# Optimization experiments

Measured on AMD Instinct MI355X. Metric: run time of the kernel, lower is better.

Reference implementation:

```python
import jax, jax.numpy as jnp
import numpy as np

BETA = 6.0
LOG_2PI = float(np.log(2.0 * np.pi))


def setup_inputs() -> dict:
    key = jax.random.key(0)
    k1, k2, k3, k4 = jax.random.split(key, 4)
    B, L = 2048, 64
    kl = jax.random.uniform(k1, (B, L), dtype=jnp.float32)
    z_mean = jax.random.normal(k2, (B, L), dtype=jnp.float32)
    z_logvar = jax.random.normal(k3, (B, L), dtype=jnp.float32)
    z_sampled = jax.random.normal(k4, (B, L), dtype=jnp.float32)
    return {"kl": kl, "z_mean": z_mean, "z_logvar": z_logvar, "z_sampled": z_sampled}


def gaussian_log_density(samples, mean, log_var):
    # samples: [B,1,L], mean/log_var: [1,B,L] -> [B,B,L]
    tmp = samples - mean
    return -0.5 * (tmp * tmp * jnp.exp(-log_var) + log_var + LOG_2PI)


def total_correlation(z, z_mean, z_logvar):
    # [B, B, L]: log q(z_i_l | x_j)
    log_qz_prob = gaussian_log_density(z[:, None, :], z_mean[None, :, :], z_logvar[None, :, :])
    # sum_l logsumexp_j -> [B]
    log_qz_product = jnp.sum(jax.scipy.special.logsumexp(log_qz_prob, axis=1), axis=1)
    # logsumexp_j sum_l -> [B]
    log_qz = jax.scipy.special.logsumexp(jnp.sum(log_qz_prob, axis=2), axis=1)
    return jnp.mean(log_qz - log_qz_product)


def reference(kl, z_mean, z_logvar, z_sampled):
    kl_loss = jnp.sum(kl)
    tc = (BETA - 1.0) * total_correlation(z_sampled, z_mean, z_logvar)
    return tc + kl_loss
```

## Files before the change

### kernel.cpp

```cpp
#include <hip/hip_runtime.h>
#include <math.h>


#define NB 2048
#define NL 64
#define NE (NB * NL)
#define BVAL 12.0f

__device__ __forceinline__ float wredsum(float v) {
#pragma unroll
  for (int o = 32; o; o >>= 1) v += __shfl_xor(v, o, 64);
  return v;
}
__device__ __forceinline__ float wredmax(float v) {
#pragma unroll
  for (int o = 32; o; o >>= 1) v = fmaxf(v, __shfl_xor(v, o, 64));
  return v;
}

__global__ __launch_bounds__(256) void k1_pre(const float* __restrict__ kl,
                                              const float* __restrict__ zm,
                                              const float* __restrict__ zlv,
                                              float2* __restrict__ PK2A,
                                              float* __restrict__ PK2B,
                                              float* __restrict__ A2T,
                                              float* __restrict__ MA2T,
                                              float* __restrict__ QC2,
                                              float* __restrict__ KLP) {
  const float INVLN2 = 1.4426950408889634f;
  const float LOG2PI = 1.8378770664093453f;
  int tid = threadIdx.x;
  int e = blockIdx.x * 256 + tid;
  int j = e >> 6, l = e & 63;
  float lv = zlv[e], m = zm[e];
  float a2 = -0.5f * INVLN2 * __expf(-lv);
  float b2 = -0.5f * INVLN2 * (lv + LOG2PI);
  float c1 = -2.0f * a2 * m;
  float c0 = fmaf(a2 * m, m, b2);
  PK2A[e] = make_float2(a2, c1);
  PK2B[e] = c0 - BVAL;
  A2T[l * NB + j] = a2;
  MA2T[l * NB + j] = c1;
  float q = wredsum(c0);
  if (l == 0) QC2[j] = q;
  float ks = wredsum(kl[e]);
  __shared__ float sk[4];
  if (l == 0) sk[tid >> 6] = ks;
  __syncthreads();
  if (tid == 0) KLP[blockIdx.x] = sk[0] + sk[1] + sk[2] + sk[3];
}

__global__ __launch_bounds__(256) void k23(const float* __restrict__ zs,
                                           const float* __restrict__ A2T,
                                           const float* __restrict__ MA2T,
                                           const float* __restrict__ QC2,
                                           const float2* __restrict__ PK2A,
                                           const float* __restrict__ PK2B,
                                           float* __restrict__ TPM,
                                           float* __restrict__ TPS,
                                           float* __restrict__ SP) {
  int jc = blockIdx.x;
  int i0 = blockIdx.y * 8;
  int tid = threadIdx.x;
  int w = tid >> 6, l = tid & 63;
  int j = jc * 256 + tid;

  __shared__ float zsh[64][8];
  if (tid < 128) {
    int k = tid >> 1, r0 = (tid & 1) * 4;
#pragma unroll
    for (int r = 0; r < 4; ++r) zsh[k][r0 + r] = zs[(i0 + r0 + r) * NL + k];
  }
  __syncthreads();

  float accv[8];
  float q = QC2[j];
#pragma unroll
  for (int r = 0; r < 8; ++r) accv[r] = q;
  for (int k = 0; k < 64; ++k) {
    float av = A2T[k * NB + j];
    float mv = MA2T[k * NB + j];
    const float4* z4 = (const float4*)&zsh[k][0];
    float4 za = z4[0], zb = z4[1];
    float zk[8] = {za.x, za.y, za.z, za.w, zb.x, zb.y, zb.z, zb.w};
#pragma unroll
    for (int r = 0; r < 8; ++r) {
      accv[r] = fmaf(zk[r] * zk[r], av, accv[r]);
      accv[r] = fmaf(zk[r], mv, accv[r]);
    }
  }
  __shared__ float lm[4][8], ls[4][8];
  float Mt[8];
#pragma unroll
  for (int r = 0; r < 8; ++r) {
    float mx = wredmax(accv[r]);
    if (l == 0) lm[w][r] = mx;
  }
  __syncthreads();
#pragma unroll
  for (int r = 0; r < 8; ++r)
    Mt[r] = fmaxf(fmaxf(lm[0][r], lm[1][r]), fmaxf(lm[2][r], lm[3][r]));
#pragma unroll
  for (int r = 0; r < 8; ++r) {
    float ss = wredsum(__builtin_amdgcn_exp2f(accv[r] - Mt[r]));
    if (l == 0) ls[w][r] = ss;
  }
  __syncthreads();
  if (tid == 0) {
#pragma unroll
    for (int r = 0; r < 8; ++r) {
      TPM[(i0 + r) * 8 + jc] = Mt[r];
      TPS[(i0 + r) * 8 + jc] = ls[0][r] + ls[1][r] + ls[2][r] + ls[3][r];
    }
  }

  float zr[8];
#pragma unroll
  for (int r = 0; r < 8; ++r) zr[r] = zs[(i0 + r) * NL + l];
  float S[8];
#pragma unroll
  for (int r = 0; r < 8; ++r) S[r] = 0.0f;
  const float2* pa = PK2A + (size_t)(jc * 256 + w * 64) * NL + l;
  const float* pb = PK2B + (size_t)(jc * 256 + w * 64) * NL + l;
#pragma unroll 4
  for (int jj = 0; jj < 64; ++jj) {
    float2 c01 = pa[(size_t)jj * NL];
    float c2 = pb[(size_t)jj * NL];
#pragma unroll
    for (int r = 0; r < 8; ++r) {
      float lp2 = fmaf(fmaf(zr[r], c01.x, c01.y), zr[r], c2);
      S[r] += __builtin_amdgcn_exp2f(lp2);
    }
  }
  __shared__ float lss[4][8][64];
#pragma unroll
  for (int r = 0; r < 8; ++r) lss[w][r][l] = S[r];
  __syncthreads();
  for (int pp = tid; pp < 512; pp += 256) {
    int r = pp >> 6, ll = pp & 63;
    float Sc = lss[0][r][ll] + lss[1][r][ll] + lss[2][r][ll] + lss[3][r][ll];
    SP[((size_t)jc * NB + (i0 + r)) * NL + ll] = Sc;
  }
}

__global__ __launch_bounds__(256) void k4_fin(const float* __restrict__ SP,
                                              const float* __restrict__ TPM,
                                              const float* __restrict__ TPS,
                                              float* __restrict__ PERI) {
  int tid = threadIdx.x;
  int w = tid >> 6, l = tid & 63;
  int i = blockIdx.x * 4 + w;
  float S = 0.0f;
#pragma unroll
  for (int s = 0; s < 8; ++s) S += SP[((size_t)s * NB + i) * NL + l];
  float val = __builtin_amdgcn_logf(S);
  float lqp2 = wredsum(val) + 64.0f * BVAL;
  float tm = (l < 8) ? TPM[i * 8 + l] : -1e30f;
  float ts = (l < 8) ? TPS[i * 8 + l] : 0.0f;
  float Mt = wredmax(tm);
  float St = wredsum(ts * __builtin_amdgcn_exp2f(tm - Mt));
  float lqz2 = Mt + __builtin_amdgcn_logf(St);
  if (l == 0) PERI[i] = lqz2 - lqp2;
}

__global__ __launch_bounds__(256) void k5_out(const float* __restrict__ KLP,
                                              const float* __restrict__ PERI,
                                              float* __restrict__ out) {
  int tid = threadIdx.x;
  float a = 0.0f, b = 0.0f;
  for (int x = tid; x < 512; x += 256) a += KLP[x];
  for (int x = tid; x < 2048; x += 256) b += PERI[x];
  float ra = wredsum(a), rb = wredsum(b);
  __shared__ float sa[4], sb[4];
  if ((tid & 63) == 0) {
    sa[tid >> 6] = ra;
    sb[tid >> 6] = rb;
  }
  __syncthreads();
  if (tid == 0) {
    const float LN2 = 0.6931471805599453f;
    float ka = sa[0] + sa[1] + sa[2] + sa[3];
    float kb = sb[0] + sb[1] + sb[2] + sb[3];
    out[0] = ka + 5.0f * LN2 * kb * (1.0f / (float)NB);
  }
}

extern "C" void kernel_launch(void* const* d_in, const int* in_sizes, int n_in,
                              void* d_out, int out_size, void* d_ws, size_t ws_size,
                              hipStream_t stream) {
  const float* kl = (const float*)d_in[0];
  const float* zm = (const float*)d_in[1];
  const float* zlv = (const float*)d_in[2];
  const float* zs = (const float*)d_in[3];
  float* ws = (float*)d_ws;

  float* PK2A = ws;
  float* PK2B = PK2A + 2 * NE;
  float* A2T = PK2B + NE;
  float* MA2T = A2T + NE;
  float* QC2 = MA2T + NE;
  float* SP = QC2 + NB;
  float* TPM = SP + 8 * NE;
  float* TPS = TPM + NB * 8;
  float* KLP = TPS + NB * 8;
  float* PERI = KLP + 512;

  k1_pre<<<NE / 256, 256, 0, stream>>>(kl, zm, zlv, (float2*)PK2A, PK2B, A2T,
                                       MA2T, QC2, KLP);
  k23<<<dim3(8, NB / 8), 256, 0, stream>>>(zs, A2T, MA2T, QC2,
                                           (const float2*)PK2A, PK2B, TPM, TPS,
                                           SP);
  k4_fin<<<NB / 4, 256, 0, stream>>>(SP, TPM, TPS, PERI);
  k5_out<<<1, 256, 0, stream>>>(KLP, PERI, (float*)d_out);
}
```

Baseline: 130.2 us.

## Split fused k23 into two block roles and pack transposed coefficients as float2

```diff
diff --git a/kernel.cpp b/kernel.cpp
--- a/kernel.cpp
+++ b/kernel.cpp
@@ -23,8 +23,7 @@
                                               const float* __restrict__ zlv,
                                               float2* __restrict__ PK2A,
                                               float* __restrict__ PK2B,
-                                              float* __restrict__ A2T,
-                                              float* __restrict__ MA2T,
+                                              float2* __restrict__ AM2T,
                                               float* __restrict__ QC2,
                                               float* __restrict__ KLP) {
   const float INVLN2 = 1.4426950408889634f;
@@ -39,8 +38,7 @@
   float c0 = fmaf(a2 * m, m, b2);
   PK2A[e] = make_float2(a2, c1);
   PK2B[e] = c0 - BVAL;
-  A2T[l * NB + j] = a2;
-  MA2T[l * NB + j] = c1;
+  AM2T[l * NB + j] = make_float2(a2, c1);
   float q = wredsum(c0);
   if (l == 0) QC2[j] = q;
   float ks = wredsum(kl[e]);
@@ -51,8 +49,7 @@
 }
 
 __global__ __launch_bounds__(256) void k23(const float* __restrict__ zs,
-                                           const float* __restrict__ A2T,
-                                           const float* __restrict__ MA2T,
+                                           const float2* __restrict__ AM2T,
                                            const float* __restrict__ QC2,
                                            const float2* __restrict__ PK2A,
                                            const float* __restrict__ PK2B,
@@ -60,86 +57,87 @@
                                            float* __restrict__ TPS,
                                            float* __restrict__ SP) {
   int jc = blockIdx.x;
-  int i0 = blockIdx.y * 8;
+  int y = blockIdx.y;
+  int i0 = (y >> 1) * 8;
   int tid = threadIdx.x;
   int w = tid >> 6, l = tid & 63;
-  int j = jc * 256 + tid;
-
-  __shared__ float zsh[64][8];
-  if (tid < 128) {
-    int k = tid >> 1, r0 = (tid & 1) * 4;
-#pragma unroll
-    for (int r = 0; r < 4; ++r) zsh[k][r0 + r] = zs[(i0 + r0 + r) * NL + k];
-  }
-  __syncthreads();
-
-  float accv[8];
-  float q = QC2[j];
-#pragma unroll
-  for (int r = 0; r < 8; ++r) accv[r] = q;
-  for (int k = 0; k < 64; ++k) {
-    float av = A2T[k * NB + j];
-    float mv = MA2T[k * NB + j];
-    const float4* z4 = (const float4*)&zsh[k][0];
-    float4 za = z4[0], zb = z4[1];
-    float zk[8] = {za.x, za.y, za.z, za.w, zb.x, zb.y, zb.z, zb.w};
+
+  if ((y & 1) == 0) {
+    int j = jc * 256 + tid;
+    __shared__ float zsh[64][8];
+    if (tid < 128) {
+      int k = tid >> 1, r0 = (tid & 1) * 4;
+#pragma unroll
+      for (int r = 0; r < 4; ++r) zsh[k][r0 + r] = zs[(i0 + r0 + r) * NL + k];
+    }
+    __syncthreads();
+    float accv[8];
+    float q = QC2[j];
+#pragma unroll
+    for (int r = 0; r < 8; ++r) accv[r] = q;
+    for (int k = 0; k < 64; ++k) {
+      float2 am = AM2T[k * NB + j];
+      const float4* z4 = (const float4*)&zsh[k][0];
+      float4 za = z4[0], zb = z4[1];
+      float zk[8] = {za.x, za.y, za.z, za.w, zb.x, zb.y, zb.z, zb.w};
+#pragma unroll
+      for (int r = 0; r < 8; ++r) {
+        accv[r] = fmaf(zk[r] * zk[r], am.x, accv[r]);
+        accv[r] = fmaf(zk[r], am.y, accv[r]);
+      }
+    }
+    __shared__ float lm[4][8], ls[4][8];
+    float Mt[8];
 #pragma unroll
     for (int r = 0; r < 8; ++r) {
-      accv[r] = fmaf(zk[r] * zk[r], av, accv[r]);
-      accv[r] = fmaf(zk[r], mv, accv[r]);
-    }
-  }
-  __shared__ float lm[4][8], ls[4][8];
-  float Mt[8];
-#pragma unroll
-  for (int r = 0; r < 8; ++r) {
-    float mx = wredmax(accv[r]);
-    if (l == 0) lm[w][r] = mx;
-  }
-  __syncthreads();
-#pragma unroll
-  for (int r = 0; r < 8; ++r)
-    Mt[r] = fmaxf(fmaxf(lm[0][r], lm[1][r]), fmaxf(lm[2][r], lm[3][r]));
-#pragma unroll
-  for (int r = 0; r < 8; ++r) {
-    float ss = wredsum(__builtin_amdgcn_exp2f(accv[r] - Mt[r]));
-    if (l == 0) ls[w][r] = ss;
-  }
-  __syncthreads();
-  if (tid == 0) {
+      float mx = wredmax(accv[r]);
+      if (l == 0) lm[w][r] = mx;
+    }
+    __syncthreads();
+#pragma unroll
+    for (int r = 0; r < 8; ++r)
+      Mt[r] = fmaxf(fmaxf(lm[0][r], lm[1][r]), fmaxf(lm[2][r], lm[3][r]));
 #pragma unroll
     for (int r = 0; r < 8; ++r) {
-      TPM[(i0 + r) * 8 + jc] = Mt[r];
-      TPS[(i0 + r) * 8 + jc] = ls[0][r] + ls[1][r] + ls[2][r] + ls[3][r];
-    }
-  }
-
-  float zr[8];
-#pragma unroll
-  for (int r = 0; r < 8; ++r) zr[r] = zs[(i0 + r) * NL + l];
-  float S[8];
-#pragma unroll
-  for (int r = 0; r < 8; ++r) S[r] = 0.0f;
-  const float2* pa = PK2A + (size_t)(jc * 256 + w * 64) * NL + l;
-  const float* pb = PK2B + (size_t)(jc * 256 + w * 64) * NL + l;
+      float ss = wredsum(__builtin_amdgcn_exp2f(accv[r] - Mt[r]));
+      if (l == 0) ls[w][r] = ss;
+    }
+    __syncthreads();
+    if (tid == 0) {
+#pragma unroll
+      for (int r = 0; r < 8; ++r) {
+        TPM[(i0 + r) * 8 + jc] = Mt[r];
+        TPS[(i0 + r) * 8 + jc] = ls[0][r] + ls[1][r] + ls[2][r] + ls[3][r];
+      }
+    }
+  } else {
+    float zr[8];
+#pragma unroll
+    for (int r = 0; r < 8; ++r) zr[r] = zs[(i0 + r) * NL + l];
+    float S[8];
+#pragma unroll
+    for (int r = 0; r < 8; ++r) S[r] = 0.0f;
+    const float2* pa = PK2A + (size_t)(jc * 256 + w * 64) * NL + l;
+    const float* pb = PK2B + (size_t)(jc * 256 + w * 64) * NL + l;
 #pragma unroll 4
-  for (int jj = 0; jj < 64; ++jj) {
-    float2 c01 = pa[(size_t)jj * NL];
-    float c2 = pb[(size_t)jj * NL];
-#pragma unroll
-    for (int r = 0; r < 8; ++r) {
-      float lp2 = fmaf(fmaf(zr[r], c01.x, c01.y), zr[r], c2);
-      S[r] += __builtin_amdgcn_exp2f(lp2);
-    }
-  }
-  __shared__ float lss[4][8][64];
-#pragma unroll
-  for (int r = 0; r < 8; ++r) lss[w][r][l] = S[r];
-  __syncthreads();
-  for (int pp = tid; pp < 512; pp += 256) {
-    int r = pp >> 6, ll = pp & 63;
-    float Sc = lss[0][r][ll] + lss[1][r][ll] + lss[2][r][ll] + lss[3][r][ll];
-    SP[((size_t)jc * NB + (i0 + r)) * NL + ll] = Sc;
+    for (int jj = 0; jj < 64; ++jj) {
+      float2 c01 = pa[(size_t)jj * NL];
+      float c2 = pb[(size_t)jj * NL];
+#pragma unroll
+      for (int r = 0; r < 8; ++r) {
+        float lp2 = fmaf(fmaf(zr[r], c01.x, c01.y), zr[r], c2);
+        S[r] += __builtin_amdgcn_exp2f(lp2);
+      }
+    }
+    __shared__ float lss[4][8][64];
+#pragma unroll
+    for (int r = 0; r < 8; ++r) lss[w][r][l] = S[r];
+    __syncthreads();
+    for (int pp = tid; pp < 512; pp += 256) {
+      int r = pp >> 6, ll = pp & 63;
+      float Sc = lss[0][r][ll] + lss[1][r][ll] + lss[2][r][ll] + lss[3][r][ll];
+      SP[((size_t)jc * NB + (i0 + r)) * NL + ll] = Sc;
+    }
   }
 }
 
@@ -196,20 +194,19 @@
 
   float* PK2A = ws;
   float* PK2B = PK2A + 2 * NE;
-  float* A2T = PK2B + NE;
-  float* MA2T = A2T + NE;
-  float* QC2 = MA2T + NE;
+  float* AM2T = PK2B + NE;
+  float* QC2 = AM2T + 2 * NE;
   float* SP = QC2 + NB;
   float* TPM = SP + 8 * NE;
   float* TPS = TPM + NB * 8;
   float* KLP = TPS + NB * 8;
   float* PERI = KLP + 512;
 
-  k1_pre<<<NE / 256, 256, 0, stream>>>(kl, zm, zlv, (float2*)PK2A, PK2B, A2T,
-                                       MA2T, QC2, KLP);
-  k23<<<dim3(8, NB / 8), 256, 0, stream>>>(zs, A2T, MA2T, QC2,
-                                           (const float2*)PK2A, PK2B, TPM, TPS,
-                                           SP);
+  k1_pre<<<NE / 256, 256, 0, stream>>>(kl, zm, zlv, (float2*)PK2A, PK2B,
+                                       (float2*)AM2T, QC2, KLP);
+  k23<<<dim3(8, 2 * (NB / 8)), 256, 0, stream>>>(zs, (const float2*)AM2T, QC2,
+                                                 (const float2*)PK2A, PK2B,
+                                                 TPM, TPS, SP);
   k4_fin<<<NB / 4, 256, 0, stream>>>(SP, TPM, TPS, PERI);
   k5_out<<<1, 256, 0, stream>>>(KLP, PERI, (float*)d_out);
 }
```

After: 134.4 us. 1.03x slower.
